# Optimization experiments

Measured on AMD Instinct MI355X. Metric: run time of the kernel, lower is better.

## Reference

```python
import jax, jax.numpy as jnp
import numpy as np

B, N, C = 4, 2048, 768
H = 6  # 3 obj heads + 3 pose heads (forced by the chained matmul shapes)


def setup_inputs() -> dict:
    key = jax.random.key(0)
    k1, k2, k3 = jax.random.split(key, 3)
    x = jax.random.normal(k1, (B, N, C), dtype=jnp.float32)
    w_qkv = jax.random.normal(k2, (3 * C, C), dtype=jnp.float32) * (C ** -0.5)
    w_proj = jax.random.normal(k3, (C, C // 2), dtype=jnp.float32) * ((C // 2) ** -0.5)
    b_proj = jnp.zeros((C,), dtype=jnp.float32)
    return {"x": x, "w_qkv": w_qkv, "w_proj": w_proj, "b_proj": b_proj, "num_heads": H}


def reference(x, w_qkv, w_proj, b_proj, num_heads):
    b, n, c = x.shape
    hd = c // num_heads
    scale = hd ** -0.5
    # qkv projection -> [3, B, H, N, hd]
    qkv = (x @ w_qkv.T).reshape(b, n, 3, num_heads, hd)
    qkv = jnp.transpose(qkv, (2, 0, 3, 1, 4))
    q, k, v = qkv[0], qkv[1], qkv[2]
    # head split: first 3 heads -> obj (sigmoid), last 3 -> pose (softmax)
    attn_obj = jax.nn.sigmoid(jnp.einsum('bhqd,bhkd->bhqk', q[:, 0:3], k[:, 0:3]) * scale)
    attn_pose = jax.nn.softmax(jnp.einsum('bhqd,bhkd->bhqk', q[:, 3:], k[:, 3:]) * scale, axis=-1)
    # chained matmuls: (attn_pose @ (attn_obj @ v_pose))  -> [B, 3, N, hd]
    ctx = jnp.einsum('bhqk,bhkd->bhqd', attn_obj, v[:, 3:])
    ctx = jnp.einsum('bhqk,bhkd->bhqd', attn_pose, ctx)
    out = jnp.transpose(ctx, (0, 2, 1, 3)).reshape(b, n, c // 2)
    out = out @ w_proj.T + b_proj
    return out, attn_obj
```

## Files before the change

kernel.cpp:

```cpp
#include <hip/hip_runtime.h>

typedef _Float16 half8 __attribute__((ext_vector_type(8)));
typedef _Float16 half4v __attribute__((ext_vector_type(4)));
typedef float f32x4 __attribute__((ext_vector_type(4)));
typedef float f32x16 __attribute__((ext_vector_type(16)));

#define MFMA16(a, b, c) __builtin_amdgcn_mfma_f32_16x16x32_f16((a), (b), (c), 0, 0, 0)
#define MFMA32(a, b, c) __builtin_amdgcn_mfma_f32_32x32x16_f16((a), (b), (c), 0, 0, 0)
#define FENCE() __builtin_amdgcn_sched_barrier(0)
#define BAR() __builtin_amdgcn_s_barrier()

__device__ __forceinline__ void gl_lds16(const void* g, void* l) {
  __builtin_amdgcn_global_load_lds(
      (const __attribute__((address_space(1))) unsigned int*)g,
      (__attribute__((address_space(3))) unsigned int*)l, 16, 0, 0);
}

__device__ __forceinline__ unsigned pkh2(float a, float b) {
  unsigned lo = (unsigned)__builtin_bit_cast(unsigned short, (_Float16)a);
  unsigned hf = (unsigned)__builtin_bit_cast(unsigned short, (_Float16)b);
  return lo | (hf << 16);
}

__global__ __launch_bounds__(256) void k_cvt_all(const float* __restrict__ x,
                                                 const float* __restrict__ wq,
                                                 const float* __restrict__ wp,
                                                 _Float16* __restrict__ xb,
                                                 _Float16* __restrict__ wqb,
                                                 _Float16* __restrict__ wpb) {
  int i = blockIdx.x * 256 + threadIdx.x;
  const float4* src;
  half4v* dst;
  int j;
  if (i < 1572864) { src = (const float4*)x; dst = (half4v*)xb; j = i; }
  else if (i < 1572864 + 442368) { src = (const float4*)wq; dst = (half4v*)wqb; j = i - 1572864; }
  else if (i < 2088960) { src = (const float4*)wp; dst = (half4v*)wpb; j = i - 2015232; }
  else return;
  float4 v = src[j];
  half4v h;
  h[0] = (_Float16)v.x; h[1] = (_Float16)v.y;
  h[2] = (_Float16)v.z; h[3] = (_Float16)v.w;
  dst[j] = h;
}

__global__ __launch_bounds__(256) void k_qkv(const _Float16* __restrict__ A,
                                             const _Float16* __restrict__ Bt,
                                             _Float16* __restrict__ Qw,
                                             _Float16* __restrict__ Kw,
                                             _Float16* __restrict__ Vtw) {
  __shared__ _Float16 As[2][128 * 64];
  __shared__ _Float16 Bs[2][128 * 64];
  const int tid = threadIdx.x;
  const int w = tid >> 6, l = tid & 63;
  const int wr = w >> 1, wc = w & 1, hi = l >> 4;
  const int bid0 = blockIdx.x;
  const int bid = (bid0 & 7) * 144 + (bid0 >> 3);
  const int tm = bid / 18, tn = bid % 18;
  const int m0 = tm * 128, n0 = tn * 128;

  auto stage = [&](int it, int dst) {
    int k0 = it * 64;
#pragma unroll
    for (int r = 0; r < 4; ++r) {
      int seg = r * 256 + tid;
      int row = seg >> 3, cs = (seg & 7) ^ (row & 7);
      gl_lds16(A + (size_t)(m0 + row) * 768 + k0 + cs * 8, (char*)As[dst] + (r * 256 + w * 64) * 16);
      gl_lds16(Bt + (size_t)(n0 + row) * 768 + k0 + cs * 8, (char*)Bs[dst] + (r * 256 + w * 64) * 16);
    }
  };

  f32x4 acc[4][4] = {};
  stage(0, 0);
  asm volatile("s_waitcnt vmcnt(0)" ::: "memory");
  BAR();
  for (int it = 0; it < 12; ++it) {
    const int cur = it & 1;
    stage(it < 11 ? it + 1 : 11, cur ^ 1);
    asm volatile("s_waitcnt vmcnt(8)" ::: "memory");
    FENCE();
    BAR();
    FENCE();
#pragma unroll
    for (int ks = 0; ks < 2; ++ks) {
#pragma unroll
      for (int m = 0; m < 4; ++m) {
        int rowa = wr * 64 + m * 16 + (l & 15);
        half8 av = *(const half8*)&As[cur][rowa * 64 + (((ks * 4 + hi) ^ (rowa & 7)) * 8)];
#pragma unroll
        for (int n = 0; n < 4; ++n) {
          int rowb = wc * 64 + n * 16 + (l & 15);
          half8 bv = *(const half8*)&Bs[cur][rowb * 64 + (((ks * 4 + hi) ^ (rowb & 7)) * 8)];
          acc[m][n] = MFMA16(av, bv, acc[m][n]);
        }
      }
    }
    FENCE();
    BAR();
  }
  asm volatile("s_waitcnt vmcnt(0)" ::: "memory");

  const float scale = 0.08838834764831845f;
#pragma unroll
  for (int m = 0; m < 4; ++m) {
    int gmb = m0 + wr * 64 + m * 16 + ((l >> 4) << 2);
#pragma unroll
    for (int n = 0; n < 4; ++n) {
      int gn0 = n0 + wc * 64 + n * 16;
      int t = gn0 / 768, rem = gn0 % 768;
      int h = rem >> 7, d = (rem & 127) + (l & 15);
      if (t == 2) {
        int bB = gmb >> 11, ntok0 = gmb & 2047;
        half4v hv;
#pragma unroll
        for (int j = 0; j < 4; ++j) hv[j] = (_Float16)acc[m][n][j];
        *(half4v*)&Vtw[((size_t)(bB * 6 + h) * 128 + d) * 2048 + ntok0] = hv;
      } else {
#pragma unroll
        for (int j = 0; j < 4; ++j) {
          int gm = gmb + j;
          int b = gm >> 11, ntok = gm & 2047;
          float v = acc[m][n][j];
          if (t == 0)
            Qw[((size_t)(b * 6 + h) * 2048 + ntok) * 128 + d] = (_Float16)(v * scale);
          else
            Kw[((size_t)(b * 6 + h) * 2048 + ntok) * 128 + d] = (_Float16)v;
        }
      }
    }
  }
}

__global__ __launch_bounds__(256, 2) void k_obj(const _Float16* __restrict__ Qw,
                                                const _Float16* __restrict__ Kw,
                                                const _Float16* __restrict__ Vtw,
                                                float* __restrict__ attn,
                                                _Float16* __restrict__ c1t) {
  __shared__ _Float16 Ks[2][64 * 128];
  __shared__ _Float16 Vs[2][128 * 64];
  __shared__ float Ts[4][1024];
  const int tid = threadIdx.x, w = tid >> 6, l = tid & 63;
  const int wr = w >> 1, wc = w & 1, hi = l >> 5, q = l & 31;
  const int bid0 = blockIdx.x;
  const int bid = (bid0 & 7) * 48 + (bid0 >> 3);
  const int b = bid / 96, rem = bid % 96, h = rem / 32, qb = rem % 32;
  const _Float16* Qg = Qw + ((size_t)(b * 6 + h) * 2048 + qb * 64 + wr * 32) * 128;
  const _Float16* Kg = Kw + ((size_t)(b * 6 + h) * 2048) * 128;
  const _Float16* Vg = Vtw + ((size_t)(b * 6 + h + 3) * 128) * 2048;
  float* attng = attn + ((size_t)(b * 3 + h) * 2048 + qb * 64) * 2048;

  auto stagePair = [&](int t, int dstb) {
#pragma unroll
    for (int r = 0; r < 4; ++r) {
      int seg = r * 256 + tid;
      int row = seg >> 4, cs = (seg & 15) ^ (row & 7);
      gl_lds16(Kg + (size_t)(t * 64 + row) * 128 + cs * 8,
               (char*)Ks[dstb] + (r * 256 + w * 64) * 16);
      int rowv = seg >> 3, csv = (seg & 7) ^ (rowv & 7);
      gl_lds16(Vg + (size_t)rowv * 2048 + t * 64 + csv * 8,
               (char*)Vs[dstb] + (r * 256 + w * 64) * 16);
    }
  };

  half8 qreg[8];
#pragma unroll
  for (int s = 0; s < 8; ++s)
    qreg[s] = *(const half8*)&Qg[(size_t)q * 128 + s * 16 + hi * 8];
  stagePair(0, 0);
  asm volatile("s_waitcnt vmcnt(0)" ::: "memory");
  BAR();

  f32x16 acc[4] = {};
  for (int kt = 0; kt < 32; ++kt) {
    const int cur = kt & 1;
    stagePair((kt + 1) & 31, cur ^ 1);
    asm volatile("s_waitcnt vmcnt(12)" ::: "memory");
    FENCE(); BAR(); FENCE();
    f32x16 p0 = {}, p1 = {};
    const int krow = wc * 32 + q;
    __builtin_amdgcn_s_setprio(1);
#pragma unroll
    for (int s = 0; s < 4; ++s) {
      int c0 = (s * 2 + hi) ^ (krow & 7);
      half8 a0 = *(const half8*)&Ks[cur][krow * 128 + c0 * 8];
      p0 = MFMA32(a0, qreg[s], p0);
      int c1 = ((s + 4) * 2 + hi) ^ (krow & 7);
      half8 a1 = *(const half8*)&Ks[cur][krow * 128 + c1 * 8];
      p1 = MFMA32(a1, qreg[s + 4], p1);
    }
    __builtin_amdgcn_s_setprio(0);
    f32x16 p = p0 + p1;
#pragma unroll
    for (int r = 0; r < 16; ++r) p[r] = 1.0f / (1.0f + __expf(-p[r]));
    {
      float* T = Ts[w];
#pragma unroll
      for (int r = 0; r < 16; ++r) {
        int kv = (r & 3) + 8 * (r >> 2) + 4 * hi;
        T[q * 32 + (kv ^ ((q & 7) << 2))] = p[r];
      }
#pragma unroll
      for (int i = 0; i < 4; ++i) {
        int qr = (l >> 3) + 8 * i;
        int kvq = (l & 7) * 4;
        f32x4 v4 = *(const f32x4*)&T[qr * 32 + (kvq ^ ((qr & 7) << 2))];
        *(f32x4*)&attng[(size_t)(wr * 32 + qr) * 2048 + kt * 64 + wc * 32 + kvq] = v4;
      }
    }
    union { unsigned uu[4]; half8 v; } bf0, bf1;
    {
      unsigned pk01 = pkh2(p[0], p[1]), pk23 = pkh2(p[2], p[3]);
      unsigned pk45 = pkh2(p[4], p[5]), pk67 = pkh2(p[6], p[7]);
      unsigned x = hi ? pk01 : pk45, y = hi ? pk23 : pk67;
      unsigned xsw = (unsigned)__shfl_xor((int)x, 32);
      unsigned ysw = (unsigned)__shfl_xor((int)y, 32);
      bf0.uu[0] = hi ? xsw : pk01; bf0.uu[1] = hi ? ysw : pk23;
      bf0.uu[2] = hi ? pk45 : xsw; bf0.uu[3] = hi ? pk67 : ysw;
    }
    {
      unsigned pk01 = pkh2(p[8], p[9]), pk23 = pkh2(p[10], p[11]);
      unsigned pk45 = pkh2(p[12], p[13]), pk67 = pkh2(p[14], p[15]);
      unsigned x = hi ? pk01 : pk45, y = hi ? pk23 : pk67;
      unsigned xsw = (unsigned)__shfl_xor((int)x, 32);
      unsigned ysw = (unsigned)__shfl_xor((int)y, 32);
      bf1.uu[0] = hi ? xsw : pk01; bf1.uu[1] = hi ? ysw : pk23;
      bf1.uu[2] = hi ? pk45 : xsw; bf1.uu[3] = hi ? pk67 : ysw;
    }
    __builtin_amdgcn_s_setprio(1);
#pragma unroll
    for (int ks = 0; ks < 2; ++ks) {
#pragma unroll
      for (int dt = 0; dt < 4; ++dt) {
        int vrow = dt * 32 + q;
        int chunk = (wc * 4 + ks * 2 + hi) ^ (vrow & 7);
        half8 av = *(const half8*)&Vs[cur][vrow * 64 + chunk * 8];
        acc[dt] = MFMA32(av, ks ? bf1.v : bf0.v, acc[dt]);
      }
    }
    __builtin_amdgcn_s_setprio(0);
    FENCE();
    BAR();
  }
  __syncthreads();
  float* mb = (float*)Ks;
  if (wc == 1) {
#pragma unroll
    for (int dt = 0; dt < 4; ++dt)
#pragma unroll
      for (int r = 0; r < 16; ++r) {
        int d = dt * 32 + (r & 3) + 8 * (r >> 2) + 4 * hi;
        mb[(wr * 128 + d) * 32 + q] = acc[dt][r];
      }
  }
  __syncthreads();
  if (wc == 0) {
    _Float16* cg = c1t + (size_t)(b * 3 + h) * 128 * 2048;
    int n = qb * 64 + wr * 32 + q;
#pragma unroll
    for (int dt = 0; dt < 4; ++dt)
#pragma unroll
      for (int r = 0; r < 16; ++r) {
        int d = dt * 32 + (r & 3) + 8 * (r >> 2) + 4 * hi;
        cg[(size_t)d * 2048 + n] = (_Float16)(acc[dt][r] + mb[(wr * 128 + d) * 32 + q]);
      }
  }
}

__global__ __launch_bounds__(256, 2) void k_pose(const _Float16* __restrict__ Qw,
                                                 const _Float16* __restrict__ Kw,
                                                 const _Float16* __restrict__ c1t,
                                                 _Float16* __restrict__ c2) {
  __shared__ _Float16 Ks[2][64 * 128];
  __shared__ _Float16 Cs[2][128 * 64];
  __shared__ float lbuf[64];
  const int tid = threadIdx.x, w = tid >> 6, l = tid & 63;
  const int wr = w >> 1, wc = w & 1, hi = l >> 5, q = l & 31;
  const int bid0 = blockIdx.x;
  const int bid = (bid0 & 7) * 48 + (bid0 >> 3);
  const int b = bid / 96, rem = bid % 96, h = rem / 32, qb = rem % 32;
  const _Float16* Qg = Qw + ((size_t)(b * 6 + h + 3) * 2048 + qb * 64 + wr * 32) * 128;
  const _Float16* Kg = Kw + ((size_t)(b * 6 + h + 3) * 2048) * 128;
  const _Float16* Cg = c1t + ((size_t)(b * 3 + h) * 128) * 2048;

  auto stagePair = [&](int t, int dstb) {
#pragma unroll
    for (int r = 0; r < 4; ++r) {
      int seg = r * 256 + tid;
      int row = seg >> 4, cs = (seg & 15) ^ (row & 7);
      gl_lds16(Kg + (size_t)(t * 64 + row) * 128 + cs * 8,
               (char*)Ks[dstb] + (r * 256 + w * 64) * 16);
      int rowv = seg >> 3, csv = (seg & 7) ^ (rowv & 7);
      gl_lds16(Cg + (size_t)rowv * 2048 + t * 64 + csv * 8,
               (char*)Cs[dstb] + (r * 256 + w * 64) * 16);
    }
  };

  half8 qreg[8];
#pragma unroll
  for (int s = 0; s < 8; ++s)
    qreg[s] = *(const half8*)&Qg[(size_t)q * 128 + s * 16 + hi * 8];
  stagePair(0, 0);
  asm volatile("s_waitcnt vmcnt(0)" ::: "memory");
  BAR();

  f32x16 acc[4] = {};
  float lsum = 0.f;
  for (int kt = 0; kt < 32; ++kt) {
    const int cur = kt & 1;
    stagePair((kt + 1) & 31, cur ^ 1);
    asm volatile("s_waitcnt vmcnt(8)" ::: "memory");
    FENCE(); BAR(); FENCE();
    f32x16 p0 = {}, p1 = {};
    const int krow = wc * 32 + q;
    __builtin_amdgcn_s_setprio(1);
#pragma unroll
    for (int s = 0; s < 4; ++s) {
      int c0 = (s * 2 + hi) ^ (krow & 7);
      half8 a0 = *(const half8*)&Ks[cur][krow * 128 + c0 * 8];
      p0 = MFMA32(a0, qreg[s], p0);
      int c1 = ((s + 4) * 2 + hi) ^ (krow & 7);
      half8 a1 = *(const half8*)&Ks[cur][krow * 128 + c1 * 8];
      p1 = MFMA32(a1, qreg[s + 4], p1);
    }
    __builtin_amdgcn_s_setprio(0);
    f32x16 p = p0 + p1;
#pragma unroll
    for (int r = 0; r < 16; ++r) {
      p[r] = __expf(p[r]);
      lsum += p[r];
    }
    union { unsigned uu[4]; half8 v; } bf0, bf1;
    {
      unsigned pk01 = pkh2(p[0], p[1]), pk23 = pkh2(p[2], p[3]);
      unsigned pk45 = pkh2(p[4], p[5]), pk67 = pkh2(p[6], p[7]);
      unsigned x = hi ? pk01 : pk45, y = hi ? pk23 : pk67;
      unsigned xsw = (unsigned)__shfl_xor((int)x, 32);
      unsigned ysw = (unsigned)__shfl_xor((int)y, 32);
      bf0.uu[0] = hi ? xsw : pk01; bf0.uu[1] = hi ? ysw : pk23;
      bf0.uu[2] = hi ? pk45 : xsw; bf0.uu[3] = hi ? pk67 : ysw;
    }
    {
      unsigned pk01 = pkh2(p[8], p[9]), pk23 = pkh2(p[10], p[11]);
      unsigned pk45 = pkh2(p[12], p[13]), pk67 = pkh2(p[14], p[15]);
      unsigned x = hi ? pk01 : pk45, y = hi ? pk23 : pk67;
      unsigned xsw = (unsigned)__shfl_xor((int)x, 32);
      unsigned ysw = (unsigned)__shfl_xor((int)y, 32);
      bf1.uu[0] = hi ? xsw : pk01; bf1.uu[1] = hi ? ysw : pk23;
      bf1.uu[2] = hi ? pk45 : xsw; bf1.uu[3] = hi ? pk67 : ysw;
    }
    __builtin_amdgcn_s_setprio(1);
#pragma unroll
    for (int ks = 0; ks < 2; ++ks) {
#pragma unroll
      for (int dt = 0; dt < 4; ++dt) {
        int vrow = dt * 32 + q;
        int chunk = (wc * 4 + ks * 2 + hi) ^ (vrow & 7);
        half8 av = *(const half8*)&Cs[cur][vrow * 64 + chunk * 8];
        acc[dt] = MFMA32(av, ks ? bf1.v : bf0.v, acc[dt]);
      }
    }
    __builtin_amdgcn_s_setprio(0);
    FENCE();
    BAR();
  }
  __syncthreads();
  float lsum2 = lsum + (float)__shfl_xor(lsum, 32);
  float* mb = (float*)Ks;
  _Float16* ob = (_Float16*)Cs;
  if (wc == 1) {
#pragma unroll
    for (int dt = 0; dt < 4; ++dt)
#pragma unroll
      for (int r = 0; r < 16; ++r) {
        int d = dt * 32 + (r & 3) + 8 * (r >> 2) + 4 * hi;
        mb[(wr * 128 + d) * 32 + q] = acc[dt][r];
      }
    if (l < 32) lbuf[wr * 32 + q] = lsum2;
  }
  __syncthreads();
  if (wc == 0) {
    float inv = 1.0f / (lsum2 + lbuf[wr * 32 + q]);
    int qbl = wr * 32 + q;
#pragma unroll
    for (int dt = 0; dt < 4; ++dt)
#pragma unroll
      for (int g = 0; g < 4; ++g) {
        int d0 = dt * 32 + 8 * g + 4 * hi;
        float v0 = (acc[dt][4 * g + 0] + mb[(wr * 128 + d0 + 0) * 32 + q]) * inv;
        float v1 = (acc[dt][4 * g + 1] + mb[(wr * 128 + d0 + 1) * 32 + q]) * inv;
        float v2 = (acc[dt][4 * g + 2] + mb[(wr * 128 + d0 + 2) * 32 + q]) * inv;
        float v3 = (acc[dt][4 * g + 3] + mb[(wr * 128 + d0 + 3) * 32 + q]) * inv;
        union { unsigned u[2]; half4v v; } hv;
        hv.u[0] = pkh2(v0, v1);
        hv.u[1] = pkh2(v2, v3);
        int c8 = (d0 >> 2) ^ ((qbl & 7) << 2);
        *(half4v*)&ob[qbl * 128 + c8 * 4] = hv.v;
      }
  }
  __syncthreads();
  {
    _Float16* cg = c2 + ((size_t)b * 2048 + qb * 64) * 384 + h * 128;
    int qbl = tid >> 2;
#pragma unroll
    for (int j = 0; j < 4; ++j) {
      int ii = (tid & 3) + j * 4;
      int c8 = (ii * 2) ^ ((qbl & 7) << 2);
      half8 v = *(const half8*)&ob[qbl * 128 + c8 * 4];
      *(half8*)&cg[(size_t)qbl * 384 + ii * 8] = v;
    }
  }
}

__global__ __launch_bounds__(256) void k_proj(const _Float16* __restrict__ A,
                                              const _Float16* __restrict__ Bt,
                                              const float* __restrict__ bias,
                                              float* __restrict__ out) {
  __shared__ _Float16 As[2][128 * 64];
  __shared__ _Float16 Bs[2][128 * 64];
  const int tid = threadIdx.x;
  const int w = tid >> 6, l = tid & 63;
  const int wr = w >> 1, wc = w & 1, hi = l >> 4;
  const int bid0 = blockIdx.x;
  const int bid = (bid0 & 7) * 48 + (bid0 >> 3);
  const int tm = bid / 6, tn = bid % 6;
  const int m0 = tm * 128, n0 = tn * 128;

  auto stage = [&](int it, int dst) {
    int k0 = it * 64;
#pragma unroll
    for (int r = 0; r < 4; ++r) {
      int seg = r * 256 + tid;
      int row = seg >> 3, cs = (seg & 7) ^ (row & 7);
      gl_lds16(A + (size_t)(m0 + row) * 384 + k0 + cs * 8, (char*)As[dst] + (r * 256 + w * 64) * 16);
      gl_lds16(Bt + (size_t)(n0 + row) * 384 + k0 + cs * 8, (char*)Bs[dst] + (r * 256 + w * 64) * 16);
    }
  };

  f32x4 acc[4][4] = {};
  stage(0, 0);
  asm volatile("s_waitcnt vmcnt(0)" ::: "memory");
  BAR();
  for (int it = 0; it < 6; ++it) {
    const int cur = it & 1;
    stage(it < 5 ? it + 1 : 5, cur ^ 1);
    asm volatile("s_waitcnt vmcnt(8)" ::: "memory");
    FENCE();
    BAR();
    FENCE();
#pragma unroll
    for (int ks = 0; ks < 2; ++ks) {
#pragma unroll
      for (int m = 0; m < 4; ++m) {
        int rowa = wr * 64 + m * 16 + (l & 15);
        half8 av = *(const half8*)&As[cur][rowa * 64 + (((ks * 4 + hi) ^ (rowa & 7)) * 8)];
#pragma unroll
        for (int n = 0; n < 4; ++n) {
          int rowb = wc * 64 + n * 16 + (l & 15);
          half8 bv = *(const half8*)&Bs[cur][rowb * 64 + (((ks * 4 + hi) ^ (rowb & 7)) * 8)];
          acc[m][n] = MFMA16(av, bv, acc[m][n]);
        }
      }
    }
    FENCE();
    BAR();
  }
  asm volatile("s_waitcnt vmcnt(0)" ::: "memory");

#pragma unroll
  for (int m = 0; m < 4; ++m) {
    int gmb = m0 + wr * 64 + m * 16 + ((l >> 4) << 2);
#pragma unroll
    for (int n = 0; n < 4; ++n) {
      int gn = n0 + wc * 64 + n * 16 + (l & 15);
      float bv = bias[gn];
#pragma unroll
      for (int j = 0; j < 4; ++j) {
        int gm = gmb + j;
        out[(size_t)gm * 768 + gn] = acc[m][n][j] + bv;
      }
    }
  }
}

extern "C" void kernel_launch(void* const* d_in, const int* in_sizes, int n_in,
                              void* d_out, int out_size, void* d_ws, size_t ws_size,
                              hipStream_t stream) {
  const float* x = (const float*)d_in[0];
  const float* wqkv = (const float*)d_in[1];
  const float* wproj = (const float*)d_in[2];
  const float* bproj = (const float*)d_in[3];

  _Float16* xb = (_Float16*)d_ws;
  _Float16* wqkvb = xb + 6291456;
  _Float16* wprojb = wqkvb + 1769472;
  _Float16* Qw = wprojb + 294912;
  _Float16* Kw = Qw + 6291456;
  _Float16* Vtw = Kw + 6291456;
  _Float16* c1t = Vtw + 6291456;
  _Float16* c2 = c1t + 3145728;

  float* out = (float*)d_out;
  float* attn = out + 6291456;

  k_cvt_all<<<8160, 256, 0, stream>>>(x, wqkv, wproj, xb, wqkvb, wprojb);
  k_qkv<<<1152, 256, 0, stream>>>(xb, wqkvb, Qw, Kw, Vtw);
  k_obj<<<384, 256, 0, stream>>>(Qw, Kw, Vtw, attn, c1t);
  k_pose<<<384, 256, 0, stream>>>(Qw, Kw, c1t, c2);
  k_proj<<<384, 256, 0, stream>>>(c2, wprojb, bproj, out);
}
```

Before: 213.7 us.

## Use register-staged 128-wide KV tiles in attention kernels, hoist GEMM LDS fragment loads

In the obj and pose attention kernels, the double-buffered direct global-to-LDS loads of 64-key tiles are replaced by a single LDS buffer of 128-key tiles. The next tile is prefetched into registers and written to LDS after a barrier, which halves the number of barriers per key sweep but adds many VGPRs. The attn writeback now happens after the PV MFMAs. In the QKV and output GEMMs, all A/B fragments are loaded from LDS before the MFMA burst, which runs under raised priority. The extra register pressure could lower occupancy or cause spills.

New measurement: 224.3 us. 5.0% more time.

```diff
diff --git a/kernel.cpp b/kernel.cpp
--- a/kernel.cpp
+++ b/kernel.cpp
@@ -4,6 +4,7 @@
 typedef _Float16 half4v __attribute__((ext_vector_type(4)));
 typedef float f32x4 __attribute__((ext_vector_type(4)));
 typedef float f32x16 __attribute__((ext_vector_type(16)));
+typedef unsigned int u32x4 __attribute__((ext_vector_type(4)));
 
 #define MFMA16(a, b, c) __builtin_amdgcn_mfma_f32_16x16x32_f16((a), (b), (c), 0, 0, 0)
 #define MFMA32(a, b, c) __builtin_amdgcn_mfma_f32_32x32x16_f16((a), (b), (c), 0, 0, 0)
@@ -80,20 +81,25 @@
     FENCE();
     BAR();
     FENCE();
-#pragma unroll
-    for (int ks = 0; ks < 2; ++ks) {
-#pragma unroll
-      for (int m = 0; m < 4; ++m) {
-        int rowa = wr * 64 + m * 16 + (l & 15);
-        half8 av = *(const half8*)&As[cur][rowa * 64 + (((ks * 4 + hi) ^ (rowa & 7)) * 8)];
-#pragma unroll
-        for (int n = 0; n < 4; ++n) {
-          int rowb = wc * 64 + n * 16 + (l & 15);
-          half8 bv = *(const half8*)&Bs[cur][rowb * 64 + (((ks * 4 + hi) ^ (rowb & 7)) * 8)];
-          acc[m][n] = MFMA16(av, bv, acc[m][n]);
-        }
-      }
-    }
+    half8 af[2][4], bf[2][4];
+#pragma unroll
+    for (int ks = 0; ks < 2; ++ks)
+#pragma unroll
+      for (int i = 0; i < 4; ++i) {
+        int rowa = wr * 64 + i * 16 + (l & 15);
+        af[ks][i] = *(const half8*)&As[cur][rowa * 64 + (((ks * 4 + hi) ^ (rowa & 7)) * 8)];
+        int rowb = wc * 64 + i * 16 + (l & 15);
+        bf[ks][i] = *(const half8*)&Bs[cur][rowb * 64 + (((ks * 4 + hi) ^ (rowb & 7)) * 8)];
+      }
+    __builtin_amdgcn_s_setprio(1);
+#pragma unroll
+    for (int ks = 0; ks < 2; ++ks)
+#pragma unroll
+      for (int m = 0; m < 4; ++m)
+#pragma unroll
+        for (int n = 0; n < 4; ++n)
+          acc[m][n] = MFMA16(af[ks][m], bf[ks][n], acc[m][n]);
+    __builtin_amdgcn_s_setprio(0);
     FENCE();
     BAR();
   }
@@ -135,8 +141,8 @@
                                                 const _Float16* __restrict__ Vtw,
                                                 float* __restrict__ attn,
                                                 _Float16* __restrict__ c1t) {
-  __shared__ _Float16 Ks[2][64 * 128];
-  __shared__ _Float16 Vs[2][128 * 64];
+  __shared__ _Float16 Ks[128 * 128];
+  __shared__ _Float16 Vs[128 * 128];
   __shared__ float Ts[4][1024];
   const int tid = threadIdx.x, w = tid >> 6, l = tid & 63;
   const int wr = w >> 1, wc = w & 1, hi = l >> 5, q = l & 31;
@@ -148,95 +154,109 @@
   const _Float16* Vg = Vtw + ((size_t)(b * 6 + h + 3) * 128) * 2048;
   float* attng = attn + ((size_t)(b * 3 + h) * 2048 + qb * 64) * 2048;
 
-  auto stagePair = [&](int t, int dstb) {
-#pragma unroll
-    for (int r = 0; r < 4; ++r) {
-      int seg = r * 256 + tid;
-      int row = seg >> 4, cs = (seg & 15) ^ (row & 7);
-      gl_lds16(Kg + (size_t)(t * 64 + row) * 128 + cs * 8,
-               (char*)Ks[dstb] + (r * 256 + w * 64) * 16);
-      int rowv = seg >> 3, csv = (seg & 7) ^ (rowv & 7);
-      gl_lds16(Vg + (size_t)rowv * 2048 + t * 64 + csv * 8,
-               (char*)Vs[dstb] + (r * 256 + w * 64) * 16);
-    }
+  u32x4 kr[8], vr[8];
+  auto issueLoads = [&](int t) {
+#pragma unroll
+    for (int r = 0; r < 8; ++r) {
+      int seg = r * 256 + tid, row = seg >> 4, cs = (seg & 15) ^ (row & 7);
+      kr[r] = *(const u32x4*)(Kg + (size_t)(t * 128 + row) * 128 + cs * 8);
+    }
+#pragma unroll
+    for (int r = 0; r < 8; ++r) {
+      int seg = r * 256 + tid, row = seg >> 4, cs = (seg & 15) ^ (row & 7);
+      vr[r] = *(const u32x4*)(Vg + (size_t)row * 2048 + t * 128 + cs * 8);
+    }
+  };
+  auto writeLds = [&]() {
+#pragma unroll
+    for (int r = 0; r < 8; ++r) *(u32x4*)((char*)Ks + (r * 256 + tid) * 16) = kr[r];
+#pragma unroll
+    for (int r = 0; r < 8; ++r) *(u32x4*)((char*)Vs + (r * 256 + tid) * 16) = vr[r];
   };
 
   half8 qreg[8];
 #pragma unroll
   for (int s = 0; s < 8; ++s)
     qreg[s] = *(const half8*)&Qg[(size_t)q * 128 + s * 16 + hi * 8];
-  stagePair(0, 0);
+
+  issueLoads(0);
   asm volatile("s_waitcnt vmcnt(0)" ::: "memory");
+  FENCE();
+  writeLds();
+  issueLoads(1);
+  asm volatile("s_waitcnt lgkmcnt(0)" ::: "memory");
+  FENCE();
   BAR();
 
   f32x16 acc[4] = {};
-  for (int kt = 0; kt < 32; ++kt) {
-    const int cur = kt & 1;
-    stagePair((kt + 1) & 31, cur ^ 1);
-    asm volatile("s_waitcnt vmcnt(12)" ::: "memory");
-    FENCE(); BAR(); FENCE();
-    f32x16 p0 = {}, p1 = {};
-    const int krow = wc * 32 + q;
-    __builtin_amdgcn_s_setprio(1);
-#pragma unroll
-    for (int s = 0; s < 4; ++s) {
-      int c0 = (s * 2 + hi) ^ (krow & 7);
-      half8 a0 = *(const half8*)&Ks[cur][krow * 128 + c0 * 8];
-      p0 = MFMA32(a0, qreg[s], p0);
-      int c1 = ((s + 4) * 2 + hi) ^ (krow & 7);
-      half8 a1 = *(const half8*)&Ks[cur][krow * 128 + c1 * 8];
-      p1 = MFMA32(a1, qreg[s + 4], p1);
-    }
-    __builtin_amdgcn_s_setprio(0);
-    f32x16 p = p0 + p1;
-#pragma unroll
-    for (int r = 0; r < 16; ++r) p[r] = 1.0f / (1.0f + __expf(-p[r]));
-    {
-      float* T = Ts[w];
-#pragma unroll
-      for (int r = 0; r < 16; ++r) {
-        int kv = (r & 3) + 8 * (r >> 2) + 4 * hi;
-        T[q * 32 + (kv ^ ((q & 7) << 2))] = p[r];
-      }
-#pragma unroll
-      for (int i = 0; i < 4; ++i) {
-        int qr = (l >> 3) + 8 * i;
-        int kvq = (l & 7) * 4;
-        f32x4 v4 = *(const f32x4*)&T[qr * 32 + (kvq ^ ((qr & 7) << 2))];
-        *(f32x4*)&attng[(size_t)(wr * 32 + qr) * 2048 + kt * 64 + wc * 32 + kvq] = v4;
-      }
-    }
-    union { unsigned uu[4]; half8 v; } bf0, bf1;
-    {
-      unsigned pk01 = pkh2(p[0], p[1]), pk23 = pkh2(p[2], p[3]);
-      unsigned pk45 = pkh2(p[4], p[5]), pk67 = pkh2(p[6], p[7]);
-      unsigned x = hi ? pk01 : pk45, y = hi ? pk23 : pk67;
-      unsigned xsw = (unsigned)__shfl_xor((int)x, 32);
-      unsigned ysw = (unsigned)__shfl_xor((int)y, 32);
-      bf0.uu[0] = hi ? xsw : pk01; bf0.uu[1] = hi ? ysw : pk23;
-      bf0.uu[2] = hi ? pk45 : xsw; bf0.uu[3] = hi ? pk67 : ysw;
-    }
-    {
-      unsigned pk01 = pkh2(p[8], p[9]), pk23 = pkh2(p[10], p[11]);
-      unsigned pk45 = pkh2(p[12], p[13]), pk67 = pkh2(p[14], p[15]);
-      unsigned x = hi ? pk01 : pk45, y = hi ? pk23 : pk67;
-      unsigned xsw = (unsigned)__shfl_xor((int)x, 32);
-      unsigned ysw = (unsigned)__shfl_xor((int)y, 32);
-      bf1.uu[0] = hi ? xsw : pk01; bf1.uu[1] = hi ? ysw : pk23;
-      bf1.uu[2] = hi ? pk45 : xsw; bf1.uu[3] = hi ? pk67 : ysw;
-    }
-    __builtin_amdgcn_s_setprio(1);
-#pragma unroll
-    for (int ks = 0; ks < 2; ++ks) {
-#pragma unroll
-      for (int dt = 0; dt < 4; ++dt) {
-        int vrow = dt * 32 + q;
-        int chunk = (wc * 4 + ks * 2 + hi) ^ (vrow & 7);
-        half8 av = *(const half8*)&Vs[cur][vrow * 64 + chunk * 8];
-        acc[dt] = MFMA32(av, ks ? bf1.v : bf0.v, acc[dt]);
-      }
-    }
-    __builtin_amdgcn_s_setprio(0);
+  for (int kt = 0; kt < 16; ++kt) {
+#pragma unroll
+    for (int sub = 0; sub < 2; ++sub) {
+      const int krow = wc * 64 + sub * 32 + q;
+      f32x16 p = {};
+      __builtin_amdgcn_s_setprio(1);
+#pragma unroll
+      for (int s = 0; s < 8; ++s) {
+        int chunk = (s * 2 + hi) ^ (krow & 7);
+        half8 av = *(const half8*)&Ks[krow * 128 + chunk * 8];
+        p = MFMA32(av, qreg[s], p);
+      }
+      __builtin_amdgcn_s_setprio(0);
+#pragma unroll
+      for (int r = 0; r < 16; ++r) p[r] = 1.0f / (1.0f + __expf(-p[r]));
+      union { unsigned uu[4]; half8 v; } bf0, bf1;
+      {
+        unsigned pk01 = pkh2(p[0], p[1]), pk23 = pkh2(p[2], p[3]);
+        unsigned pk45 = pkh2(p[4], p[5]), pk67 = pkh2(p[6], p[7]);
+        unsigned x = hi ? pk01 : pk45, y = hi ? pk23 : pk67;
+        unsigned xsw = (unsigned)__shfl_xor((int)x, 32);
+        unsigned ysw = (unsigned)__shfl_xor((int)y, 32);
+        bf0.uu[0] = hi ? xsw : pk01; bf0.uu[1] = hi ? ysw : pk23;
+        bf0.uu[2] = hi ? pk45 : xsw; bf0.uu[3] = hi ? pk67 : ysw;
+      }
+      {
+        unsigned pk01 = pkh2(p[8], p[9]), pk23 = pkh2(p[10], p[11]);
+        unsigned pk45 = pkh2(p[12], p[13]), pk67 = pkh2(p[14], p[15]);
+        unsigned x = hi ? pk01 : pk45, y = hi ? pk23 : pk67;
+        unsigned xsw = (unsigned)__shfl_xor((int)x, 32);
+        unsigned ysw = (unsigned)__shfl_xor((int)y, 32);
+        bf1.uu[0] = hi ? xsw : pk01; bf1.uu[1] = hi ? ysw : pk23;
+        bf1.uu[2] = hi ? pk45 : xsw; bf1.uu[3] = hi ? pk67 : ysw;
+      }
+      __builtin_amdgcn_s_setprio(1);
+#pragma unroll
+      for (int ks = 0; ks < 2; ++ks)
+#pragma unroll
+        for (int dt = 0; dt < 4; ++dt) {
+          int vrow = dt * 32 + q;
+          int chunk = (wc * 8 + sub * 4 + ks * 2 + hi) ^ (vrow & 7);
+          half8 av = *(const half8*)&Vs[vrow * 128 + chunk * 8];
+          acc[dt] = MFMA32(av, ks ? bf1.v : bf0.v, acc[dt]);
+        }
+      __builtin_amdgcn_s_setprio(0);
+      {
+        float* T = Ts[w];
+#pragma unroll
+        for (int r = 0; r < 16; ++r) {
+          int kv = (r & 3) + 8 * (r >> 2) + 4 * hi;
+          T[q * 32 + (kv ^ ((q & 7) << 2))] = p[r];
+        }
+#pragma unroll
+        for (int i = 0; i < 4; ++i) {
+          int qr = (l >> 3) + 8 * i;
+          int kvq = (l & 7) * 4;
+          f32x4 v4 = *(const f32x4*)&T[qr * 32 + (kvq ^ ((qr & 7) << 2))];
+          *(f32x4*)&attng[(size_t)(wr * 32 + qr) * 2048 + kt * 128 + wc * 64 + sub * 32 + kvq] = v4;
+        }
+      }
+    }
+    FENCE();
+    BAR();
+    asm volatile("s_waitcnt vmcnt(8)" ::: "memory");
+    FENCE();
+    writeLds();
+    issueLoads((kt + 2) & 15);
+    asm volatile("s_waitcnt lgkmcnt(0)" ::: "memory");
     FENCE();
     BAR();
   }
@@ -269,8 +289,8 @@
                                                  const _Float16* __restrict__ Kw,
                                                  const _Float16* __restrict__ c1t,
                                                  _Float16* __restrict__ c2) {
-  __shared__ _Float16 Ks[2][64 * 128];
-  __shared__ _Float16 Cs[2][128 * 64];
+  __shared__ _Float16 Ks[128 * 128];
+  __shared__ _Float16 Cs[128 * 128];
   __shared__ float lbuf[64];
   const int tid = threadIdx.x, w = tid >> 6, l = tid & 63;
   const int wr = w >> 1, wc = w & 1, hi = l >> 5, q = l & 31;
@@ -281,84 +301,98 @@
   const _Float16* Kg = Kw + ((size_t)(b * 6 + h + 3) * 2048) * 128;
   const _Float16* Cg = c1t + ((size_t)(b * 3 + h) * 128) * 2048;
 
-  auto stagePair = [&](int t, int dstb) {
-#pragma unroll
-    for (int r = 0; r < 4; ++r) {
-      int seg = r * 256 + tid;
-      int row = seg >> 4, cs = (seg & 15) ^ (row & 7);
-      gl_lds16(Kg + (size_t)(t * 64 + row) * 128 + cs * 8,
-               (char*)Ks[dstb] + (r * 256 + w * 64) * 16);
-      int rowv = seg >> 3, csv = (seg & 7) ^ (rowv & 7);
-      gl_lds16(Cg + (size_t)rowv * 2048 + t * 64 + csv * 8,
-               (char*)Cs[dstb] + (r * 256 + w * 64) * 16);
-    }
+  u32x4 kr[8], vr[8];
+  auto issueLoads = [&](int t) {
+#pragma unroll
+    for (int r = 0; r < 8; ++r) {
+      int seg = r * 256 + tid, row = seg >> 4, cs = (seg & 15) ^ (row & 7);
+      kr[r] = *(const u32x4*)(Kg + (size_t)(t * 128 + row) * 128 + cs * 8);
+    }
+#pragma unroll
+    for (int r = 0; r < 8; ++r) {
+      int seg = r * 256 + tid, row = seg >> 4, cs = (seg & 15) ^ (row & 7);
+      vr[r] = *(const u32x4*)(Cg + (size_t)row * 2048 + t * 128 + cs * 8);
+    }
+  };
+  auto writeLds = [&]() {
+#pragma unroll
+    for (int r = 0; r < 8; ++r) *(u32x4*)((char*)Ks + (r * 256 + tid) * 16) = kr[r];
+#pragma unroll
+    for (int r = 0; r < 8; ++r) *(u32x4*)((char*)Cs + (r * 256 + tid) * 16) = vr[r];
   };
 
   half8 qreg[8];
 #pragma unroll
   for (int s = 0; s < 8; ++s)
     qreg[s] = *(const half8*)&Qg[(size_t)q * 128 + s * 16 + hi * 8];
-  stagePair(0, 0);
+
+  issueLoads(0);
   asm volatile("s_waitcnt vmcnt(0)" ::: "memory");
+  FENCE();
+  writeLds();
+  issueLoads(1);
+  asm volatile("s_waitcnt lgkmcnt(0)" ::: "memory");
+  FENCE();
   BAR();
 
   f32x16 acc[4] = {};
   float lsum = 0.f;
-  for (int kt = 0; kt < 32; ++kt) {
-    const int cur = kt & 1;
-    stagePair((kt + 1) & 31, cur ^ 1);
-    asm volatile("s_waitcnt vmcnt(8)" ::: "memory");
-    FENCE(); BAR(); FENCE();
-    f32x16 p0 = {}, p1 = {};
-    const int krow = wc * 32 + q;
-    __builtin_amdgcn_s_setprio(1);
-#pragma unroll
-    for (int s = 0; s < 4; ++s) {
-      int c0 = (s * 2 + hi) ^ (krow & 7);
-      half8 a0 = *(const half8*)&Ks[cur][krow * 128 + c0 * 8];
-      p0 = MFMA32(a0, qreg[s], p0);
-      int c1 = ((s + 4) * 2 + hi) ^ (krow & 7);
-      half8 a1 = *(const half8*)&Ks[cur][krow * 128 + c1 * 8];
-      p1 = MFMA32(a1, qreg[s + 4], p1);
-    }
-    __builtin_amdgcn_s_setprio(0);
-    f32x16 p = p0 + p1;
-#pragma unroll
-    for (int r = 0; r < 16; ++r) {
-      p[r] = __expf(p[r]);
-      lsum += p[r];
-    }
-    union { unsigned uu[4]; half8 v; } bf0, bf1;
-    {
-      unsigned pk01 = pkh2(p[0], p[1]), pk23 = pkh2(p[2], p[3]);
-      unsigned pk45 = pkh2(p[4], p[5]), pk67 = pkh2(p[6], p[7]);
-      unsigned x = hi ? pk01 : pk45, y = hi ? pk23 : pk67;
-      unsigned xsw = (unsigned)__shfl_xor((int)x, 32);
-      unsigned ysw = (unsigned)__shfl_xor((int)y, 32);
-      bf0.uu[0] = hi ? xsw : pk01; bf0.uu[1] = hi ? ysw : pk23;
-      bf0.uu[2] = hi ? pk45 : xsw; bf0.uu[3] = hi ? pk67 : ysw;
-    }
-    {
-      unsigned pk01 = pkh2(p[8], p[9]), pk23 = pkh2(p[10], p[11]);
-      unsigned pk45 = pkh2(p[12], p[13]), pk67 = pkh2(p[14], p[15]);
-      unsigned x = hi ? pk01 : pk45, y = hi ? pk23 : pk67;
-      unsigned xsw = (unsigned)__shfl_xor((int)x, 32);
-      unsigned ysw = (unsigned)__shfl_xor((int)y, 32);
-      bf1.uu[0] = hi ? xsw : pk01; bf1.uu[1] = hi ? ysw : pk23;
-      bf1.uu[2] = hi ? pk45 : xsw; bf1.uu[3] = hi ? pk67 : ysw;
-    }
-    __builtin_amdgcn_s_setprio(1);
-#pragma unroll
-    for (int ks = 0; ks < 2; ++ks) {
-#pragma unroll
-      for (int dt = 0; dt < 4; ++dt) {
-        int vrow = dt * 32 + q;
-        int chunk = (wc * 4 + ks * 2 + hi) ^ (vrow & 7);
-        half8 av = *(const half8*)&Cs[cur][vrow * 64 + chunk * 8];
-        acc[dt] = MFMA32(av, ks ? bf1.v : bf0.v, acc[dt]);
-      }
-    }
-    __builtin_amdgcn_s_setprio(0);
+  for (int kt = 0; kt < 16; ++kt) {
+#pragma unroll
+    for (int sub = 0; sub < 2; ++sub) {
+      const int krow = wc * 64 + sub * 32 + q;
+      f32x16 p = {};
+      __builtin_amdgcn_s_setprio(1);
+#pragma unroll
+      for (int s = 0; s < 8; ++s) {
+        int chunk = (s * 2 + hi) ^ (krow & 7);
+        half8 av = *(const half8*)&Ks[krow * 128 + chunk * 8];
+        p = MFMA32(av, qreg[s], p);
+      }
+      __builtin_amdgcn_s_setprio(0);
+#pragma unroll
+      for (int r = 0; r < 16; ++r) {
+        p[r] = __expf(p[r]);
+        lsum += p[r];
+      }
+      union { unsigned uu[4]; half8 v; } bf0, bf1;
+      {
+        unsigned pk01 = pkh2(p[0], p[1]), pk23 = pkh2(p[2], p[3]);
+        unsigned pk45 = pkh2(p[4], p[5]), pk67 = pkh2(p[6], p[7]);
+        unsigned x = hi ? pk01 : pk45, y = hi ? pk23 : pk67;
+        unsigned xsw = (unsigned)__shfl_xor((int)x, 32);
+        unsigned ysw = (unsigned)__shfl_xor((int)y, 32);
+        bf0.uu[0] = hi ? xsw : pk01; bf0.uu[1] = hi ? ysw : pk23;
+        bf0.uu[2] = hi ? pk45 : xsw; bf0.uu[3] = hi ? pk67 : ysw;
+      }
+      {
+        unsigned pk01 = pkh2(p[8], p[9]), pk23 = pkh2(p[10], p[11]);
+        unsigned pk45 = pkh2(p[12], p[13]), pk67 = pkh2(p[14], p[15]);
+        unsigned x = hi ? pk01 : pk45, y = hi ? pk23 : pk67;
+        unsigned xsw = (unsigned)__shfl_xor((int)x, 32);
+        unsigned ysw = (unsigned)__shfl_xor((int)y, 32);
+        bf1.uu[0] = hi ? xsw : pk01; bf1.uu[1] = hi ? ysw : pk23;
+        bf1.uu[2] = hi ? pk45 : xsw; bf1.uu[3] = hi ? pk67 : ysw;
+      }
+      __builtin_amdgcn_s_setprio(1);
+#pragma unroll
+      for (int ks = 0; ks < 2; ++ks)
+#pragma unroll
+        for (int dt = 0; dt < 4; ++dt) {
+          int vrow = dt * 32 + q;
+          int chunk = (wc * 8 + sub * 4 + ks * 2 + hi) ^ (vrow & 7);
+          half8 av = *(const half8*)&Cs[vrow * 128 + chunk * 8];
+          acc[dt] = MFMA32(av, ks ? bf1.v : bf0.v, acc[dt]);
+        }
+      __builtin_amdgcn_s_setprio(0);
+    }
+    FENCE();
+    BAR();
+    asm volatile("s_waitcnt vmcnt(0)" ::: "memory");
+    FENCE();
+    writeLds();
+    issueLoads((kt + 2) & 15);
+    asm volatile("s_waitcnt lgkmcnt(0)" ::: "memory");
     FENCE();
     BAR();
   }
@@ -446,20 +480,25 @@
     FENCE();
     BAR();
     FENCE();
-#pragma unroll
-    for (int ks = 0; ks < 2; ++ks) {
-#pragma unroll
-      for (int m = 0; m < 4; ++m) {
-        int rowa = wr * 64 + m * 16 + (l & 15);
-        half8 av = *(const half8*)&As[cur][rowa * 64 + (((ks * 4 + hi) ^ (rowa & 7)) * 8)];
-#pragma unroll
-        for (int n = 0; n < 4; ++n) {
-          int rowb = wc * 64 + n * 16 + (l & 15);
-          half8 bv = *(const half8*)&Bs[cur][rowb * 64 + (((ks * 4 + hi) ^ (rowb & 7)) * 8)];
-          acc[m][n] = MFMA16(av, bv, acc[m][n]);
-        }
-      }
-    }
+    half8 af[2][4], bf[2][4];
+#pragma unroll
+    for (int ks = 0; ks < 2; ++ks)
+#pragma unroll
+      for (int i = 0; i < 4; ++i) {
+        int rowa = wr * 64 + i * 16 + (l & 15);
+        af[ks][i] = *(const half8*)&As[cur][rowa * 64 + (((ks * 4 + hi) ^ (rowa & 7)) * 8)];
+        int rowb = wc * 64 + i * 16 + (l & 15);
+        bf[ks][i] = *(const half8*)&Bs[cur][rowb * 64 + (((ks * 4 + hi) ^ (rowb & 7)) * 8)];
+      }
+    __builtin_amdgcn_s_setprio(1);
+#pragma unroll
+    for (int ks = 0; ks < 2; ++ks)
+#pragma unroll
+      for (int m = 0; m < 4; ++m)
+#pragma unroll
+        for (int n = 0; n < 4; ++n)
+          acc[m][n] = MFMA16(af[ks][m], bf[ks][n], acc[m][n]);
+    __builtin_amdgcn_s_setprio(0);
     FENCE();
     BAR();
   }
```

## Fuse fp32-to-fp16 conversion of x into QKV GEMM and hoist fragment loads

Applied to the files above, without the earlier changes.

The separate conversion pass over x is removed. The QKV GEMM now stages fp32 x tiles directly into LDS and converts them to fp16 in registers before the MFMAs, with the K-tile halved to 32 to fit LDS and a new swizzle for B. In both the QKV and projection GEMMs, all A/B fragments are loaded before a batch of MFMAs, and s_setprio raises wave priority during compute. This avoids writing and re-reading a 12MB fp16 copy of x, at the cost of twice as many barrier iterations and more LDS traffic per element for the fp32 A tile.

After: 230.5 us. 7.9% more time.

```diff
diff --git a/kernel.cpp b/kernel.cpp
--- a/kernel.cpp
+++ b/kernel.cpp
@@ -22,19 +22,16 @@
   return lo | (hf << 16);
 }
 
-__global__ __launch_bounds__(256) void k_cvt_all(const float* __restrict__ x,
-                                                 const float* __restrict__ wq,
-                                                 const float* __restrict__ wp,
-                                                 _Float16* __restrict__ xb,
-                                                 _Float16* __restrict__ wqb,
-                                                 _Float16* __restrict__ wpb) {
+__global__ __launch_bounds__(256) void k_cvt_w(const float* __restrict__ wq,
+                                               const float* __restrict__ wp,
+                                               _Float16* __restrict__ wqb,
+                                               _Float16* __restrict__ wpb) {
   int i = blockIdx.x * 256 + threadIdx.x;
   const float4* src;
   half4v* dst;
   int j;
-  if (i < 1572864) { src = (const float4*)x; dst = (half4v*)xb; j = i; }
-  else if (i < 1572864 + 442368) { src = (const float4*)wq; dst = (half4v*)wqb; j = i - 1572864; }
-  else if (i < 2088960) { src = (const float4*)wp; dst = (half4v*)wpb; j = i - 2015232; }
+  if (i < 442368) { src = (const float4*)wq; dst = (half4v*)wqb; j = i; }
+  else if (i < 516096) { src = (const float4*)wp; dst = (half4v*)wpb; j = i - 442368; }
   else return;
   float4 v = src[j];
   half4v h;
@@ -43,13 +40,13 @@
   dst[j] = h;
 }
 
-__global__ __launch_bounds__(256) void k_qkv(const _Float16* __restrict__ A,
-                                             const _Float16* __restrict__ Bt,
-                                             _Float16* __restrict__ Qw,
-                                             _Float16* __restrict__ Kw,
-                                             _Float16* __restrict__ Vtw) {
-  __shared__ _Float16 As[2][128 * 64];
-  __shared__ _Float16 Bs[2][128 * 64];
+__global__ __launch_bounds__(256, 3) void k_qkv(const float* __restrict__ A,
+                                                const _Float16* __restrict__ Bt,
+                                                _Float16* __restrict__ Qw,
+                                                _Float16* __restrict__ Kw,
+                                                _Float16* __restrict__ Vtw) {
+  __shared__ float Asf[2][128 * 32];
+  __shared__ _Float16 Bs[2][128 * 32];
   const int tid = threadIdx.x;
   const int w = tid >> 6, l = tid & 63;
   const int wr = w >> 1, wc = w & 1, hi = l >> 4;
@@ -59,13 +56,20 @@
   const int m0 = tm * 128, n0 = tn * 128;
 
   auto stage = [&](int it, int dst) {
-    int k0 = it * 64;
+    int k0 = it * 32;
 #pragma unroll
     for (int r = 0; r < 4; ++r) {
       int seg = r * 256 + tid;
       int row = seg >> 3, cs = (seg & 7) ^ (row & 7);
-      gl_lds16(A + (size_t)(m0 + row) * 768 + k0 + cs * 8, (char*)As[dst] + (r * 256 + w * 64) * 16);
-      gl_lds16(Bt + (size_t)(n0 + row) * 768 + k0 + cs * 8, (char*)Bs[dst] + (r * 256 + w * 64) * 16);
+      gl_lds16(A + (size_t)(m0 + row) * 768 + k0 + cs * 4,
+               (char*)Asf[dst] + (r * 256 + w * 64) * 16);
+    }
+#pragma unroll
+    for (int r = 0; r < 2; ++r) {
+      int seg = r * 256 + tid;
+      int row = seg >> 2, cs = (seg & 3) ^ ((row >> 1) & 3);
+      gl_lds16(Bt + (size_t)(n0 + row) * 768 + k0 + cs * 8,
+               (char*)Bs[dst] + (r * 256 + w * 64) * 16);
     }
   };
 
@@ -73,27 +77,35 @@
   stage(0, 0);
   asm volatile("s_waitcnt vmcnt(0)" ::: "memory");
   BAR();
-  for (int it = 0; it < 12; ++it) {
+  for (int it = 0; it < 24; ++it) {
     const int cur = it & 1;
-    stage(it < 11 ? it + 1 : 11, cur ^ 1);
-    asm volatile("s_waitcnt vmcnt(8)" ::: "memory");
+    stage(it < 23 ? it + 1 : 23, cur ^ 1);
+    asm volatile("s_waitcnt vmcnt(6)" ::: "memory");
     FENCE();
     BAR();
     FENCE();
-#pragma unroll
-    for (int ks = 0; ks < 2; ++ks) {
-#pragma unroll
-      for (int m = 0; m < 4; ++m) {
-        int rowa = wr * 64 + m * 16 + (l & 15);
-        half8 av = *(const half8*)&As[cur][rowa * 64 + (((ks * 4 + hi) ^ (rowa & 7)) * 8)];
-#pragma unroll
-        for (int n = 0; n < 4; ++n) {
-          int rowb = wc * 64 + n * 16 + (l & 15);
-          half8 bv = *(const half8*)&Bs[cur][rowb * 64 + (((ks * 4 + hi) ^ (rowb & 7)) * 8)];
-          acc[m][n] = MFMA16(av, bv, acc[m][n]);
-        }
-      }
-    }
+    half8 af[4], bfr[4];
+#pragma unroll
+    for (int i = 0; i < 4; ++i) {
+      int rowa = wr * 64 + i * 16 + (l & 15);
+      f32x4 fa = *(const f32x4*)&Asf[cur][rowa * 32 + (((2 * hi) ^ (rowa & 7)) * 4)];
+      f32x4 fb = *(const f32x4*)&Asf[cur][rowa * 32 + (((2 * hi + 1) ^ (rowa & 7)) * 4)];
+      half8 h;
+      h[0] = (_Float16)fa[0]; h[1] = (_Float16)fa[1];
+      h[2] = (_Float16)fa[2]; h[3] = (_Float16)fa[3];
+      h[4] = (_Float16)fb[0]; h[5] = (_Float16)fb[1];
+      h[6] = (_Float16)fb[2]; h[7] = (_Float16)fb[3];
+      af[i] = h;
+      int rowb = wc * 64 + i * 16 + (l & 15);
+      bfr[i] = *(const half8*)&Bs[cur][rowb * 32 + ((hi ^ ((rowb >> 1) & 3)) * 8)];
+    }
+    __builtin_amdgcn_s_setprio(1);
+#pragma unroll
+    for (int m = 0; m < 4; ++m)
+#pragma unroll
+      for (int n = 0; n < 4; ++n)
+        acc[m][n] = MFMA16(af[m], bfr[n], acc[m][n]);
+    __builtin_amdgcn_s_setprio(0);
     FENCE();
     BAR();
   }
@@ -446,20 +458,25 @@
     FENCE();
     BAR();
     FENCE();
-#pragma unroll
-    for (int ks = 0; ks < 2; ++ks) {
-#pragma unroll
-      for (int m = 0; m < 4; ++m) {
-        int rowa = wr * 64 + m * 16 + (l & 15);
-        half8 av = *(const half8*)&As[cur][rowa * 64 + (((ks * 4 + hi) ^ (rowa & 7)) * 8)];
-#pragma unroll
-        for (int n = 0; n < 4; ++n) {
-          int rowb = wc * 64 + n * 16 + (l & 15);
-          half8 bv = *(const half8*)&Bs[cur][rowb * 64 + (((ks * 4 + hi) ^ (rowb & 7)) * 8)];
-          acc[m][n] = MFMA16(av, bv, acc[m][n]);
-        }
-      }
-    }
+    half8 af[2][4], bf[2][4];
+#pragma unroll
+    for (int ks = 0; ks < 2; ++ks)
+#pragma unroll
+      for (int i = 0; i < 4; ++i) {
+        int rowa = wr * 64 + i * 16 + (l & 15);
+        af[ks][i] = *(const half8*)&As[cur][rowa * 64 + (((ks * 4 + hi) ^ (rowa & 7)) * 8)];
+        int rowb = wc * 64 + i * 16 + (l & 15);
+        bf[ks][i] = *(const half8*)&Bs[cur][rowb * 64 + (((ks * 4 + hi) ^ (rowb & 7)) * 8)];
+      }
+    __builtin_amdgcn_s_setprio(1);
+#pragma unroll
+    for (int ks = 0; ks < 2; ++ks)
+#pragma unroll
+      for (int m = 0; m < 4; ++m)
+#pragma unroll
+        for (int n = 0; n < 4; ++n)
+          acc[m][n] = MFMA16(af[ks][m], bf[ks][n], acc[m][n]);
+    __builtin_amdgcn_s_setprio(0);
     FENCE();
     BAR();
   }
@@ -489,8 +506,7 @@
   const float* wproj = (const float*)d_in[2];
   const float* bproj = (const float*)d_in[3];
 
-  _Float16* xb = (_Float16*)d_ws;
-  _Float16* wqkvb = xb + 6291456;
+  _Float16* wqkvb = (_Float16*)d_ws;
   _Float16* wprojb = wqkvb + 1769472;
   _Float16* Qw = wprojb + 294912;
   _Float16* Kw = Qw + 6291456;
@@ -501,8 +517,8 @@
   float* out = (float*)d_out;
   float* attn = out + 6291456;
 
-  k_cvt_all<<<8160, 256, 0, stream>>>(x, wqkv, wproj, xb, wqkvb, wprojb);
-  k_qkv<<<1152, 256, 0, stream>>>(xb, wqkvb, Qw, Kw, Vtw);
+  k_cvt_w<<<2016, 256, 0, stream>>>(wqkv, wproj, wqkvb, wprojb);
+  k_qkv<<<1152, 256, 0, stream>>>(x, wqkvb, Qw, Kw, Vtw);
   k_obj<<<384, 256, 0, stream>>>(Qw, Kw, Vtw, attn, c1t);
   k_pose<<<384, 256, 0, stream>>>(Qw, Kw, c1t, c2);
   k_proj<<<384, 256, 0, stream>>>(c2, wprojb, bproj, out);
```

## Stage transposed V and c1t stores through LDS; hoist fragment loads in GEMMs

Applied to the files above, without the earlier changes.

The V-part of the QKV GEMM epilogue and the c1t epilogue of the obj kernel now transpose their tiles in shared memory, using padded strides. They then write 16-byte coalesced rows to global memory instead of scattered 8-byte or 2-byte stores. The QKV and projection GEMM inner loops load all A/B fragments for the K-step into registers before a contiguous MFMA burst, raising wave priority during the MFMAs. These changes cost extra barriers and LDS reuse, and the preloaded fragments raise register pressure.

After: 210.3 us. Within noise of the previous version (-1.6%).

```diff
diff --git a/kernel.cpp b/kernel.cpp
--- a/kernel.cpp
+++ b/kernel.cpp
@@ -48,8 +48,7 @@
                                              _Float16* __restrict__ Qw,
                                              _Float16* __restrict__ Kw,
                                              _Float16* __restrict__ Vtw) {
-  __shared__ _Float16 As[2][128 * 64];
-  __shared__ _Float16 Bs[2][128 * 64];
+  __shared__ _Float16 AB[4][128 * 64];
   const int tid = threadIdx.x;
   const int w = tid >> 6, l = tid & 63;
   const int wr = w >> 1, wc = w & 1, hi = l >> 4;
@@ -64,8 +63,10 @@
     for (int r = 0; r < 4; ++r) {
       int seg = r * 256 + tid;
       int row = seg >> 3, cs = (seg & 7) ^ (row & 7);
-      gl_lds16(A + (size_t)(m0 + row) * 768 + k0 + cs * 8, (char*)As[dst] + (r * 256 + w * 64) * 16);
-      gl_lds16(Bt + (size_t)(n0 + row) * 768 + k0 + cs * 8, (char*)Bs[dst] + (r * 256 + w * 64) * 16);
+      gl_lds16(A + (size_t)(m0 + row) * 768 + k0 + cs * 8,
+               (char*)AB[dst] + (r * 256 + w * 64) * 16);
+      gl_lds16(Bt + (size_t)(n0 + row) * 768 + k0 + cs * 8,
+               (char*)AB[2 + dst] + (r * 256 + w * 64) * 16);
     }
   };
 
@@ -80,41 +81,65 @@
     FENCE();
     BAR();
     FENCE();
-#pragma unroll
-    for (int ks = 0; ks < 2; ++ks) {
-#pragma unroll
-      for (int m = 0; m < 4; ++m) {
-        int rowa = wr * 64 + m * 16 + (l & 15);
-        half8 av = *(const half8*)&As[cur][rowa * 64 + (((ks * 4 + hi) ^ (rowa & 7)) * 8)];
-#pragma unroll
-        for (int n = 0; n < 4; ++n) {
-          int rowb = wc * 64 + n * 16 + (l & 15);
-          half8 bv = *(const half8*)&Bs[cur][rowb * 64 + (((ks * 4 + hi) ^ (rowb & 7)) * 8)];
-          acc[m][n] = MFMA16(av, bv, acc[m][n]);
-        }
-      }
-    }
+    half8 af[2][4], bfr[2][4];
+#pragma unroll
+    for (int ks = 0; ks < 2; ++ks)
+#pragma unroll
+      for (int i = 0; i < 4; ++i) {
+        int rowa = wr * 64 + i * 16 + (l & 15);
+        af[ks][i] = *(const half8*)&AB[cur][rowa * 64 + (((ks * 4 + hi) ^ (rowa & 7)) * 8)];
+        int rowb = wc * 64 + i * 16 + (l & 15);
+        bfr[ks][i] = *(const half8*)&AB[2 + cur][rowb * 64 + (((ks * 4 + hi) ^ (rowb & 7)) * 8)];
+      }
+    __builtin_amdgcn_s_setprio(1);
+#pragma unroll
+    for (int ks = 0; ks < 2; ++ks)
+#pragma unroll
+      for (int m = 0; m < 4; ++m)
+#pragma unroll
+        for (int n = 0; n < 4; ++n)
+          acc[m][n] = MFMA16(af[ks][m], bfr[ks][n], acc[m][n]);
+    __builtin_amdgcn_s_setprio(0);
     FENCE();
     BAR();
   }
   asm volatile("s_waitcnt vmcnt(0)" ::: "memory");
 
   const float scale = 0.08838834764831845f;
-#pragma unroll
-  for (int m = 0; m < 4; ++m) {
-    int gmb = m0 + wr * 64 + m * 16 + ((l >> 4) << 2);
-#pragma unroll
-    for (int n = 0; n < 4; ++n) {
-      int gn0 = n0 + wc * 64 + n * 16;
-      int t = gn0 / 768, rem = gn0 % 768;
-      int h = rem >> 7, d = (rem & 127) + (l & 15);
-      if (t == 2) {
-        int bB = gmb >> 11, ntok0 = gmb & 2047;
+  if (tn >= 12) {
+    __syncthreads();
+    _Float16* vt = AB[0];
+#pragma unroll
+    for (int m = 0; m < 4; ++m)
+#pragma unroll
+      for (int n = 0; n < 4; ++n) {
+        int dl = wc * 64 + n * 16 + (l & 15);
+        int tl = wr * 64 + m * 16 + ((l >> 4) << 2);
         half4v hv;
 #pragma unroll
         for (int j = 0; j < 4; ++j) hv[j] = (_Float16)acc[m][n][j];
-        *(half4v*)&Vtw[((size_t)(bB * 6 + h) * 128 + d) * 2048 + ntok0] = hv;
-      } else {
+        *(half4v*)&vt[dl * 136 + tl] = hv;
+      }
+    __syncthreads();
+    const int h = tn - 12;
+    const int bB = m0 >> 11, nt0 = m0 & 2047;
+    _Float16* vg = Vtw + ((size_t)(bB * 6 + h) * 128) * 2048 + nt0;
+    int lr = tid & 15, dr0 = tid >> 4;
+#pragma unroll
+    for (int itp = 0; itp < 8; ++itp) {
+      int d = dr0 + itp * 16;
+      half8 v = *(const half8*)&vt[d * 136 + lr * 8];
+      *(half8*)&vg[(size_t)d * 2048 + lr * 8] = v;
+    }
+  } else {
+#pragma unroll
+    for (int m = 0; m < 4; ++m) {
+      int gmb = m0 + wr * 64 + m * 16 + ((l >> 4) << 2);
+#pragma unroll
+      for (int n = 0; n < 4; ++n) {
+        int gn0 = n0 + wc * 64 + n * 16;
+        int t = gn0 / 768, rem = gn0 % 768;
+        int h = rem >> 7, d = (rem & 127) + (l & 15);
 #pragma unroll
         for (int j = 0; j < 4; ++j) {
           int gm = gmb + j;
@@ -242,6 +267,7 @@
   }
   __syncthreads();
   float* mb = (float*)Ks;
+  _Float16* ct = (_Float16*)Vs;
   if (wc == 1) {
 #pragma unroll
     for (int dt = 0; dt < 4; ++dt)
@@ -253,15 +279,25 @@
   }
   __syncthreads();
   if (wc == 0) {
-    _Float16* cg = c1t + (size_t)(b * 3 + h) * 128 * 2048;
-    int n = qb * 64 + wr * 32 + q;
+    int nl = wr * 32 + q;
 #pragma unroll
     for (int dt = 0; dt < 4; ++dt)
 #pragma unroll
       for (int r = 0; r < 16; ++r) {
         int d = dt * 32 + (r & 3) + 8 * (r >> 2) + 4 * hi;
-        cg[(size_t)d * 2048 + n] = (_Float16)(acc[dt][r] + mb[(wr * 128 + d) * 32 + q]);
-      }
+        ct[d * 76 + nl] = (_Float16)(acc[dt][r] + mb[(wr * 128 + d) * 32 + q]);
+      }
+  }
+  __syncthreads();
+  {
+    _Float16* cg = c1t + (size_t)(b * 3 + h) * 128 * 2048 + qb * 64;
+    int lr = tid & 7, dr0 = tid >> 3;
+#pragma unroll
+    for (int itp = 0; itp < 4; ++itp) {
+      int d = dr0 + itp * 32;
+      half8 v = *(const half8*)&ct[d * 76 + lr * 8];
+      *(half8*)&cg[(size_t)d * 2048 + lr * 8] = v;
+    }
   }
 }
 
@@ -446,20 +482,25 @@
     FENCE();
     BAR();
     FENCE();
-#pragma unroll
-    for (int ks = 0; ks < 2; ++ks) {
-#pragma unroll
-      for (int m = 0; m < 4; ++m) {
-        int rowa = wr * 64 + m * 16 + (l & 15);
-        half8 av = *(const half8*)&As[cur][rowa * 64 + (((ks * 4 + hi) ^ (rowa & 7)) * 8)];
-#pragma unroll
-        for (int n = 0; n < 4; ++n) {
-          int rowb = wc * 64 + n * 16 + (l & 15);
-          half8 bv = *(const half8*)&Bs[cur][rowb * 64 + (((ks * 4 + hi) ^ (rowb & 7)) * 8)];
-          acc[m][n] = MFMA16(av, bv, acc[m][n]);
-        }
-      }
-    }
+    half8 af[2][4], bf[2][4];
+#pragma unroll
+    for (int ks = 0; ks < 2; ++ks)
+#pragma unroll
+      for (int i = 0; i < 4; ++i) {
+        int rowa = wr * 64 + i * 16 + (l & 15);
+        af[ks][i] = *(const half8*)&As[cur][rowa * 64 + (((ks * 4 + hi) ^ (rowa & 7)) * 8)];
+        int rowb = wc * 64 + i * 16 + (l & 15);
+        bf[ks][i] = *(const half8*)&Bs[cur][rowb * 64 + (((ks * 4 + hi) ^ (rowb & 7)) * 8)];
+      }
+    __builtin_amdgcn_s_setprio(1);
+#pragma unroll
+    for (int ks = 0; ks < 2; ++ks)
+#pragma unroll
+      for (int m = 0; m < 4; ++m)
+#pragma unroll
+        for (int n = 0; n < 4; ++n)
+          acc[m][n] = MFMA16(af[ks][m], bf[ks][n], acc[m][n]);
+    __builtin_amdgcn_s_setprio(0);
     FENCE();
     BAR();
   }
```
